# Performance work log

Hardware: AMD Instinct MI355X
Metric: run time of the kernel (lower is better)

Reference implementation:

```python
import jax, jax.numpy as jnp
import numpy as np

N_QUBIT = 22
N_LAYERS = 2
D_LOGICAL = 2  # num_logical_dim (one logical qubit)
DIM = 2 ** N_QUBIT


def _apply_ry(psi, th, q):
    # psi: (B, 2^n) complex64; Ry(th) on qubit q (q=0 is the most significant bit)
    half = th * 0.5
    c = jnp.cos(half).astype(jnp.complex64)
    s = jnp.sin(half).astype(jnp.complex64)
    psi4 = psi.reshape(psi.shape[0], 2 ** q, 2, -1)
    p0, p1 = psi4[:, :, 0], psi4[:, :, 1]
    out = jnp.stack([c * p0 - s * p1, s * p0 + c * p1], axis=2)
    return out.reshape(psi.shape)


def _apply_cnot(psi, c, t):
    a, b = (c, t) if c < t else (t, c)
    right = 2 ** (N_QUBIT - b - 1)
    mid = 2 ** (b - a - 1)
    psi6 = psi.reshape(psi.shape[0], 2 ** a, 2, mid, 2, right)
    if c < t:
        # control is axis 2; flip target axis 4 where control==1
        psi6 = psi6.at[:, :, 1, :, :, :].set(psi6[:, :, 1, :, ::-1, :])
    else:
        # control is axis 4; flip target axis 2 where control==1
        psi6 = psi6.at[:, :, :, :, 1, :].set(psi6[:, :, ::-1, :, 1, :])
    return psi6.reshape(psi.shape)


def _apply_pauli(psi, p, q):
    psi4 = psi.reshape(psi.shape[0], 2 ** q, 2, -1)
    p0, p1 = psi4[:, :, 0], psi4[:, :, 1]
    if p == 'X':
        out = jnp.stack([p1, p0], axis=2)
    elif p == 'Y':
        out = jnp.stack([-1j * p1, 1j * p0], axis=2)
    else:  # Z
        out = jnp.stack([p0, -p1], axis=2)
    return out.reshape(psi.shape)


def _encode(theta):
    # q0[i, i] = 1 for the logical basis states, then run the circuit
    psi = jnp.zeros((D_LOGICAL, DIM), jnp.complex64)
    psi = psi.at[jnp.arange(D_LOGICAL), jnp.arange(D_LOGICAL)].set(1.0)
    for l in range(N_LAYERS):
        for q in range(N_QUBIT):
            psi = _apply_ry(psi, theta[l, q], q)
        for q in range(N_QUBIT):
            psi = _apply_cnot(psi, q, (q + 1) % N_QUBIT)
    return psi


def _kl_loss(theta):
    psi = _encode(theta)  # (D_LOGICAL, 2^n)
    # Knill-Laflamme inner products T_e[i,j] = <psi_i| E_e |psi_j> for all weight-1 Paulis
    Ts = []
    for q in range(N_QUBIT):
        for p in ('X', 'Y', 'Z'):
            epsi = _apply_pauli(psi, p, q)
            Ts.append(jnp.einsum('is,js->ij', psi.conj(), epsi))
    T = jnp.stack(Ts)  # (3*N_QUBIT, D_LOGICAL, D_LOGICAL)
    diag = jnp.diagonal(T, axis1=1, axis2=2)
    lam = diag.mean(axis=1)  # per-error lambda_e
    res = T - lam[:, None, None] * jnp.eye(D_LOGICAL, dtype=T.dtype)
    # loss_type == 'L2'
    return jnp.sum(jnp.abs(res) ** 2)


def setup_inputs() -> dict:
    key = jax.random.key(0)
    theta = jax.random.normal(key, (N_LAYERS, N_QUBIT), dtype=jnp.float32)
    return {"theta": theta}


def reference(theta):
    return _kl_loss(theta)
```

## Files before the change

### kernel.cpp

```cpp
#include <hip/hip_runtime.h>

#define NQ 22
#define DIMN (1u << NQ)

#define PG_OFF 0u
#define PM_OFF 6144u
#define PL_OFF 14336u
#define PF_OFF 126976u
#define CNT_OFF 135168u

struct MaskSet {
    unsigned L[NQ];
    unsigned Linv[NQ];
    unsigned xm[NQ];
    unsigned zm[NQ];
    unsigned frowHi[5];
};

constexpr MaskSet buildMasks() {
    MaskSet M{};
    for (int b = 0; b < NQ; ++b) M.L[b] = 1u << b;
    for (int q = 0; q < NQ; ++q) {
        int bc = NQ - 1 - q, bt = NQ - 1 - ((q + 1) % NQ);
        M.L[bt] ^= M.L[bc];
    }
    unsigned mat[NQ] = {}, aug[NQ] = {};
    for (int b = 0; b < NQ; ++b) { mat[b] = M.L[b]; aug[b] = 1u << b; }
    for (int col = 0; col < NQ; ++col) {
        int piv = col;
        while (!((mat[piv] >> col) & 1u)) ++piv;
        unsigned tm = mat[piv]; mat[piv] = mat[col]; mat[col] = tm;
        unsigned ta = aug[piv]; aug[piv] = aug[col]; aug[col] = ta;
        for (int r = 0; r < NQ; ++r)
            if (r != col && ((mat[r] >> col) & 1u)) { mat[r] ^= mat[col]; aug[r] ^= aug[col]; }
    }
    for (int b = 0; b < NQ; ++b) M.Linv[b] = aug[b];
    for (int j = 0; j < NQ; ++j) {
        int b = NQ - 1 - j;
        unsigned xmv = 0;
        for (int r = 0; r < NQ; ++r)
            if ((aug[r] >> b) & 1u) xmv |= 1u << r;
        M.xm[j] = xmv;
        M.zm[j] = M.L[b];
    }
    for (int j = 0; j < 5; ++j) {
        unsigned f = 0;
        for (int r = 0; r < NQ; ++r)
            if ((aug[r] >> (17 + j)) & 1u) f |= 1u << r;
        M.frowHi[j] = f;
    }
    return M;
}
constexpr int topbit_c(unsigned v) { int b = 0; while (v >> (b + 1)) ++b; return b; }
constexpr unsigned unionHi() {
    MaskSet M = buildMasks();
    unsigned u = 0;
    for (int j = 0; j < 5; ++j) u |= M.frowHi[j];
    return u;
}
static_assert((unionHi() & 0xFFFFu) == 0, "frowHi must only touch bits 16..21");

constexpr unsigned orbGen(int which) {
    MaskSet M = buildMasks();
    return (which == 0 ? M.xm[0] : which == 1 ? M.xm[4] : M.xm[9]) >> 2;
}
constexpr int orbS21() {
    MaskSet M = buildMasks();
    unsigned GA = M.xm[0] >> 2, GB = M.xm[4] >> 2, GC = M.xm[9] >> 2;
    unsigned GQ = M.xm[21] >> 2;
    for (int s = 1; s < 8; ++s) {
        unsigned c = ((s & 1) ? GA : 0u) ^ ((s & 2) ? GB : 0u) ^ ((s & 4) ? GC : 0u);
        if (c == GQ) return s;
    }
    return -1;
}
constexpr bool orbitOK() {
    unsigned GA = orbGen(0), GB = orbGen(1), GC = orbGen(2);
    int cA = topbit_c(GA), cB = topbit_c(GB), cC = topbit_c(GC);
    if (!(cC < cB && cB < cA) || cA > 19) return false;
    if (((GA >> cB) & 1u) || ((GA >> cC) & 1u)) return false;
    if (((GB >> cA) & 1u) || ((GB >> cC) & 1u)) return false;
    if (((GC >> cA) & 1u) || ((GC >> cB) & 1u)) return false;
    return orbS21() > 0;
}
static_assert(orbitOK(), "orbit structure for fused slice measurement must hold");

constexpr bool lowPlanOK() {
    MaskSet M = buildMasks();
    if ((M.xm[10] & ~0xE00u) != 0) return false;
    if ((M.xm[11] & ~0xE00u) != 0) return false;
    for (int q = 12; q <= 19; ++q) {
        if ((M.xm[q] & 3u) != 0 && (M.xm[q] & 3u) != 2u) return false;
        if ((M.zm[q] & 3u) != 0) return false;
        if (topbit_c(M.xm[q]) < 2 || topbit_c(M.xm[q]) > 9) return false;
    }
    if (M.xm[20] != 3u) return false;
    if ((M.zm[20] & 3u) != 2u) return false;
    return true;
}
static_assert(lowPlanOK(), "k_low measurement plan must hold");

__device__ __forceinline__ float fflip(float v, unsigned sbit31) {
    return __int_as_float(__float_as_int(v) ^ (int)sbit31);
}
__device__ __forceinline__ unsigned ph4(unsigned g) { return g ^ ((g >> 6) & 3u); }

__device__ __forceinline__ unsigned sA(unsigned i) {
    return i ^ ((i >> 3) & 7u) ^ (((i >> 6) & 3u) << 3);
}

__device__ __forceinline__ float fold4(float a, float b, float c, float d, int lane) {
    bool p0 = (lane & 1) != 0;
    float kL = p0 ? b : a, sL = p0 ? a : b;
    kL += __shfl_xor(sL, 1);
    float kH = p0 ? d : c, sH = p0 ? c : d;
    kH += __shfl_xor(sH, 1);
    bool p1 = (lane & 2) != 0;
    float k2 = p1 ? kH : kL, s2 = p1 ? kL : kH;
    k2 += __shfl_xor(s2, 2);
    k2 += __shfl_xor(k2, 4);
    k2 += __shfl_xor(k2, 8);
    k2 += __shfl_xor(k2, 16);
    k2 += __shfl_xor(k2, 32);
    return k2;
}

__device__ __forceinline__ void buildTrig(float* trig, const float* __restrict__ theta, int t) {
    if (t < 2 * NQ) {
        int l = t / NQ, q = t % NQ, b = NQ - 1 - q;
        float h = 0.5f * theta[t];
        trig[l * 2 * NQ + b]      = cosf(h);
        trig[l * 2 * NQ + NQ + b] = sinf(h);
    }
}

__device__ __forceinline__ void gates3(float* a, float* b, const float* trig, int b0) {
#pragma unroll
    for (int g = 0; g < 3; ++g) {
        float c = trig[2 * NQ + b0 + g], s = trig[3 * NQ + b0 + g];
#pragma unroll
        for (int e = 0; e < 8; ++e) {
            if (!(e & (1 << g))) {
                int e1 = e | (1 << g);
                float x0 = a[e], x1 = a[e1];
                a[e] = c * x0 - s * x1; a[e1] = s * x0 + c * x1;
                float y0 = b[e], y1 = b[e1];
                b[e] = c * y0 - s * y1; b[e1] = s * y0 + c * y1;
            }
        }
    }
}

__device__ __forceinline__ int slotOf(int s) {
    if (s < 12)  return 4 + s;
    if (s < 28)  return 8 + s;
    if (s < 248) {
        int r = (s - 28) >> 1;
        return (r < 44) ? (40 + r) : (88 + (r - 44));
    }
    int j = s - 248;
    const int b4[4] = { 0, 16, 36, 84 };
    return b4[j >> 2] + (j & 3);
}

__global__ __launch_bounds__(256, 1) void k_genHi(float* __restrict__ phi,
                                                  const float* __restrict__ theta,
                                                  float* __restrict__ P) {
    constexpr MaskSet M = buildMasks();
    __shared__ float red[4 * 12];
    __shared__ float trig[4 * NQ];
    if (blockIdx.x == 0 && threadIdx.x == 0) *(int*)(P + CNT_OFF) = 0;
    buildTrig(trig, theta, threadIdx.x);
    __syncthreads();
    unsigned base = blockIdx.x * 256u + threadIdx.x;
    unsigned P0 = 0;
#pragma unroll
    for (int b = 0; b < NQ; ++b)
        P0 |= ((unsigned)__popc(base & M.Linv[b]) & 1u) << b;
    float pc = 1.f;
#pragma unroll
    for (int b = 1; b < 16; ++b) {
        float cvb = trig[b], svb = trig[NQ + b];
        pc *= ((P0 >> b) & 1u) ? svb : cvb;
    }
    float cv0 = trig[0], sv0 = trig[NQ];
    float C0 = pc * ((P0 & 1u) ? sv0 : cv0);
    float C1 = pc * ((P0 & 1u) ? cv0 : -sv0);
    float cb[6], sb[6];
#pragma unroll
    for (int k = 0; k < 6; ++k) { cb[k] = trig[16 + k]; sb[k] = trig[NQ + 16 + k]; }
    unsigned u0 = P0 >> 16;
    float v0[32], v1[32];
#pragma unroll
    for (int e = 0; e < 32; ++e) {
        unsigned F = 0;
        if (e & 1)  F ^= M.frowHi[0];
        if (e & 2)  F ^= M.frowHi[1];
        if (e & 4)  F ^= M.frowHi[2];
        if (e & 8)  F ^= M.frowHi[3];
        if (e & 16) F ^= M.frowHi[4];
        unsigned u = u0 ^ (F >> 16);
        float vp = (u & 1u) ? sb[0] : cb[0];
#pragma unroll
        for (int k = 1; k < 6; ++k) vp *= ((u >> k) & 1u) ? sb[k] : cb[k];
        v0[e] = vp * C0;
        v1[e] = vp * C1;
    }
    float c2[5], s2[5];
#pragma unroll
    for (int j = 0; j < 5; ++j) {
        c2[j] = trig[2 * NQ + 17 + j];
        s2[j] = trig[3 * NQ + 17 + j];
    }
#pragma unroll
    for (int j = 0; j < 5; ++j) {
#pragma unroll
        for (int e = 0; e < 32; ++e) {
            if (!(e & (1 << j))) {
                int e1 = e | (1 << j);
                float a0 = v0[e], a1 = v0[e1];
                v0[e]  = c2[j] * a0 - s2[j] * a1;
                v0[e1] = s2[j] * a0 + c2[j] * a1;
                float b0 = v1[e], b1 = v1[e1];
                v1[e]  = c2[j] * b0 - s2[j] * b1;
                v1[e1] = s2[j] * b0 + c2[j] * b1;
            }
        }
    }
#pragma unroll
    for (int e = 0; e < 32; ++e) {
        unsigned a = base | ((unsigned)e << 17);
        phi[a] = v0[e];
        phi[DIMN + a] = v1[e];
    }
    int lane = threadIdx.x & 63, w = threadIdx.x >> 6;
#pragma unroll
    for (int i = 1; i <= 3; ++i) {
        unsigned ex  = M.xm[i] >> 17;
        unsigned zme = M.zm[i] >> 17;
        float t00 = 0.f, t11 = 0.f, t01 = 0.f, u01 = 0.f;
#pragma unroll
        for (int e = 0; e < 32; ++e) {
            int ep = e ^ (int)ex;
            t00 += v0[e] * v0[ep];
            t11 += v1[e] * v1[ep];
            float p = v0[e] * v1[ep];
            t01 += p;
            unsigned sg = ((unsigned)__popc((unsigned)ep & zme) & 1u) << 31;
            u01 += fflip(p, sg);
        }
        float r = fold4(t00, t11, t01, u01, lane);
        if (lane < 4) red[w * 12 + (i - 1) * 4 + lane] = r;
    }
    __syncthreads();
    int t = threadIdx.x;
    if (t < 12) {
        float r = red[t] + red[12 + t] + red[24 + t] + red[36 + t];
        P[PG_OFF + (unsigned)t * 512u + blockIdx.x] = r;
    }
}

__global__ __launch_bounds__(256, 1) void k_midA(float* __restrict__ phi,
                                                 const float* __restrict__ theta,
                                                 float* __restrict__ P) {
    constexpr MaskSet M = buildMasks();
    __shared__ float red[4 * 16];
    __shared__ float trig[4 * NQ];
    buildTrig(trig, theta, threadIdx.x);
    __syncthreads();
    unsigned tid = blockIdx.x * 256u + threadIdx.x;
    unsigned base = (tid & 0xFFFu) | ((tid >> 12) << 17);
    float v0[32], v1[32];
#pragma unroll
    for (int e = 0; e < 32; ++e) {
        unsigned a = base | ((unsigned)e << 12);
        v0[e] = phi[a];
        v1[e] = phi[DIMN + a];
    }
    float c[5], s[5];
#pragma unroll
    for (int j = 0; j < 5; ++j) {
        c[j] = trig[2 * NQ + 12 + j];
        s[j] = trig[3 * NQ + 12 + j];
    }
#pragma unroll
    for (int j = 0; j < 5; ++j) {
#pragma unroll
        for (int e = 0; e < 32; ++e) {
            if (!(e & (1 << j))) {
                int e1 = e | (1 << j);
                float a0 = v0[e], a1 = v0[e1];
                v0[e]  = c[j] * a0 - s[j] * a1;
                v0[e1] = s[j] * a0 + c[j] * a1;
                float b0 = v1[e], b1 = v1[e1];
                v1[e]  = c[j] * b0 - s[j] * b1;
                v1[e1] = s[j] * b0 + c[j] * b1;
            }
        }
    }
#pragma unroll
    for (int e = 0; e < 32; ++e) {
        unsigned a = base | ((unsigned)e << 12);
        phi[a] = v0[e];
        phi[DIMN + a] = v1[e];
    }
    int lane = threadIdx.x & 63, w = threadIdx.x >> 6;
#pragma unroll
    for (int i = 5; i <= 8; ++i) {
        unsigned ex  = (M.xm[i] >> 12) & 31u;
        unsigned zme = (M.zm[i] >> 12) & 31u;
        unsigned bs31 = ((unsigned)__popc(base & M.zm[i]) & 1u) << 31;
        float t00 = 0.f, t11 = 0.f, t01 = 0.f, u01 = 0.f;
#pragma unroll
        for (int e = 0; e < 32; ++e) {
            int ep = e ^ (int)ex;
            t00 += v0[e] * v0[ep];
            t11 += v1[e] * v1[ep];
            float p = v0[e] * v1[ep];
            t01 += p;
            unsigned sg = ((unsigned)__popc((unsigned)ep & zme) & 1u) << 31;
            u01 += fflip(p, sg ^ bs31);
        }
        float r = fold4(t00, t11, t01, u01, lane);
        if (lane < 4) red[w * 16 + (i - 5) * 4 + lane] = r;
    }
    __syncthreads();
    int t = threadIdx.x;
    if (t < 16) {
        float r = red[t] + red[16 + t] + red[32 + t] + red[48 + t];
        P[PM_OFF + (unsigned)t * 512u + blockIdx.x] = r;
    }
}

__global__ __launch_bounds__(512, 4) void k_low(float* __restrict__ phi,
                                                const float* __restrict__ theta,
                                                float* __restrict__ P) {
    constexpr MaskSet M = buildMasks();
    __shared__ float As[4096];
    __shared__ float Bs[4096];
    __shared__ float redZ[8 * 33];
    __shared__ float redQ[8 * 44];
    __shared__ float trig[4 * NQ];
    float4* As4 = (float4*)As;
    float4* Bs4 = (float4*)Bs;
    int t = threadIdx.x;
    int lane = t & 63, w = t >> 6;
    unsigned base = blockIdx.x * 4096u;
    float a[8], b[8];
    buildTrig(trig, theta, t);

    {
        const float4* g0 = (const float4*)(phi + base);
        const float4* g1 = (const float4*)(phi + DIMN + base);
        float4 va0 = g0[2 * t], va1 = g0[2 * t + 1];
        float4 vb0 = g1[2 * t], vb1 = g1[2 * t + 1];
        a[0] = va0.x; a[1] = va0.y; a[2] = va0.z; a[3] = va0.w;
        a[4] = va1.x; a[5] = va1.y; a[6] = va1.z; a[7] = va1.w;
        b[0] = vb0.x; b[1] = vb0.y; b[2] = vb0.z; b[3] = vb0.w;
        b[4] = vb1.x; b[5] = vb1.y; b[6] = vb1.z; b[7] = vb1.w;
        __syncthreads();
        gates3(a, b, trig, 0);
#pragma unroll
        for (int j = 0; j < 8; ++j) {
            unsigned i = ((unsigned)t << 3) | (unsigned)j;
            unsigned A = sA(i);
            As[A] = a[j]; Bs[A] = b[j];
        }
    }
    __syncthreads();

    {
#pragma unroll
        for (int j = 0; j < 8; ++j) {
            unsigned i = (((unsigned)t >> 3) << 6) | ((unsigned)j << 3) | ((unsigned)t & 7u);
            unsigned A = sA(i);
            a[j] = As[A]; b[j] = Bs[A];
        }
        gates3(a, b, trig, 3);
#pragma unroll
        for (int j = 0; j < 8; ++j) {
            unsigned i = (((unsigned)t >> 3) << 6) | ((unsigned)j << 3) | ((unsigned)t & 7u);
            unsigned A = sA(i);
            As[A] = a[j]; Bs[A] = b[j];
        }
    }
    __syncthreads();

    {
#pragma unroll
        for (int j = 0; j < 8; ++j) {
            unsigned i = (((unsigned)t >> 6) << 9) | ((unsigned)j << 6) | ((unsigned)t & 63u);
            unsigned A = sA(i);
            a[j] = As[A]; b[j] = Bs[A];
        }
        gates3(a, b, trig, 6);
#pragma unroll
        for (int j = 0; j < 8; ++j) {
            unsigned i = (((unsigned)t >> 6) << 9) | ((unsigned)j << 6) | ((unsigned)t & 63u);
            unsigned A = sA(i);
            As[A] = a[j]; Bs[A] = b[j];
        }
    }
    __syncthreads();

    {
#pragma unroll
        for (int j = 0; j < 8; ++j) {
            unsigned i = ((unsigned)j << 9) | (unsigned)t;
            unsigned A = sA(i);
            a[j] = As[A]; b[j] = Bs[A];
        }
        gates3(a, b, trig, 9);
    }
    __syncthreads();

#pragma unroll
    for (int j = 0; j < 8; ++j) {
        unsigned i = ((unsigned)j << 9) | (unsigned)t;
        phi[base + i] = a[j];
        phi[DIMN + base + i] = b[j];
        unsigned p = i ^ (((i >> 8) & 3u) << 2);
        As[p] = a[j]; Bs[p] = b[j];
    }

#pragma unroll
    for (int c = 0; c < 3; ++c) {
        float p[8];
#pragma unroll
        for (int j = 0; j < 8; ++j)
            p[j] = (c == 0) ? a[j] * a[j] : (c == 1) ? b[j] * b[j] : a[j] * b[j];
        float s1[4], d1[4];
#pragma unroll
        for (int j = 0; j < 4; ++j) { s1[j] = p[j] + p[j + 4]; d1[j] = p[j] - p[j + 4]; }
        float s2_0 = s1[0] + s1[2], s2_1 = s1[1] + s1[3];
        float d2_0 = d1[0] - d1[2], d2_1 = d1[1] - d1[3];
        float SS = s2_0 + s2_1;
        float z0 = (d1[0] + d1[1]) + (d1[2] + d1[3]);
        float z1 = d2_0 + d2_1;
        float d3 = d2_0 - d2_1;
        float r = fold4(SS, z0, z1, 0.f, lane);
        if (lane < 3) redZ[w * 33 + c * 11 + lane] = r;
        float v = d3;
#pragma unroll
        for (int s = 0; s < 6; ++s) {
            float u = __shfl_xor(v, 1 << s);
            v = u + fflip(v, ((unsigned)(lane >> s) & 1u) << 31);
        }
        int pcnt = __popc(lane);
        if (lane == 64 - (64 >> pcnt)) redZ[w * 33 + c * 11 + 3 + pcnt] = v;
    }
    __syncthreads();

    if (t < 66) {
        int c = t % 3, q = t / 3;
        int idx, wm;
        if (q == 0 || q == 21)      { idx = 9; wm = 7; }
        else if (q <= 9)            { idx = 0; wm = 0; }
        else if (q == 10)           { idx = 1; wm = 0; }
        else if (q == 11)           { idx = 2; wm = 0; }
        else if (q == 12)           { idx = 3; wm = 0; }
        else if (q == 13)           { idx = 3; wm = 4; }
        else if (q == 14)           { idx = 3; wm = 6; }
        else if (q == 15)           { idx = 3; wm = 7; }
        else                        { idx = q - 12; wm = 7; }
        float val = 0.f;
#pragma unroll
        for (int ww = 0; ww < 8; ++ww) {
            float rv = redZ[ww * 33 + c * 11 + idx];
            val += ((__popc(ww & wm) & 1) ? -rv : rv);
        }
        unsigned sg = (unsigned)__popc(base & M.zm[q]) & 1u;
        P[PL_OFF + (44u + (unsigned)t) * 1024u + blockIdx.x] = sg ? -val : val;
    }

#pragma unroll
    for (int i = 0; i < 2; ++i) {
        int q = 10 + i;
        unsigned je  = (M.xm[q] >> 9) & 7u;
        unsigned zmj = (M.zm[q] >> 9) & 7u;
        unsigned zb31 = ((unsigned)__popc(base & M.zm[q]) & 1u) << 31;
        float t00 = 0.f, t11 = 0.f, t01 = 0.f, u01 = 0.f;
#pragma unroll
        for (int j = 0; j < 8; ++j) {
            int jp = j ^ (int)je;
            t00 += a[j] * a[jp];
            t11 += b[j] * b[jp];
            float p = a[j] * b[jp];
            t01 += p;
            unsigned sg = ((unsigned)__popc((unsigned)jp & zmj) & 1u) << 31;
            u01 += fflip(p, sg ^ zb31);
        }
        float r = fold4(t00, t11, t01, u01, lane);
        if (lane < 4) redQ[w * 44 + 4 * i + lane] = r;
    }

#pragma unroll
    for (int iq = 2; iq < 10; ++iq) {
        int q = 10 + iq;
        unsigned m = M.xm[q], zm = M.zm[q];
        unsigned zb = (unsigned)__popc(base & zm) & 1u;
        int gb = topbit_c(M.xm[q]) - 2;
        unsigned mg4 = m >> 2;
        unsigned swap2 = m & 3u;
        float t00 = 0.f, t11 = 0.f, t01 = 0.f, u01 = 0.f;
        unsigned gc = (unsigned)t;
        unsigned g = ((gc >> gb) << (gb + 1)) | (gc & ((1u << gb) - 1u));
        unsigned gx = g ^ mg4;
        float4 a0 = As4[ph4(g)],  a1 = Bs4[ph4(g)];
        float4 b0 = As4[ph4(gx)], b1 = Bs4[ph4(gx)];
        if (swap2) {
            b0 = make_float4(b0.z, b0.w, b0.x, b0.y);
            b1 = make_float4(b1.z, b1.w, b1.x, b1.y);
        }
        unsigned szg = ((unsigned)__popc((g << 2) & zm) + zb) & 1u;
        unsigned szx = ((unsigned)__popc((gx << 2) & zm) + zb) & 1u;
        unsigned fg = szg << 31, fx = szx << 31;
        const float* A0 = &a0.x; const float* A1 = &a1.x;
        const float* B0 = &b0.x; const float* B1 = &b1.x;
#pragma unroll
        for (int j = 0; j < 4; ++j) {
            t00 += A0[j] * B0[j];
            t11 += A1[j] * B1[j];
            float p = A0[j] * B1[j], r2 = B0[j] * A1[j];
            t01 += p + r2;
            u01 += fflip(p, fx) + fflip(r2, fg);
        }
        t00 *= 2.f; t11 *= 2.f;
        float r = fold4(t00, t11, t01, u01, lane);
        if (lane < 4) redQ[w * 44 + 4 * iq + lane] = r;
    }
    {
        unsigned zm = M.zm[20];
        unsigned zb = (unsigned)__popc(base & zm) & 1u;
        float t00 = 0.f, t11 = 0.f, t01 = 0.f, u01 = 0.f;
#pragma unroll
        for (int k = 0; k < 2; ++k) {
            unsigned g = (unsigned)t + 512u * k;
            float4 a0 = As4[ph4(g)], a1 = Bs4[ph4(g)];
            unsigned szg = ((unsigned)__popc((g << 2) & zm) + zb) & 1u;
            const float* A0 = &a0.x; const float* A1 = &a1.x;
#pragma unroll
            for (int j = 0; j < 4; ++j) {
                int jx = j ^ 3;
                float p = A0[j] * A0[jx];
                float q2 = A1[j] * A1[jx];
                float cr = A0[j] * A1[jx];
                t00 += p; t11 += q2; t01 += cr;
                unsigned sj = ((unsigned)(jx >> 1) & 1u) ^ szg;
                u01 += fflip(cr, sj << 31);
            }
        }
        float r = fold4(t00, t11, t01, u01, lane);
        if (lane < 4) redQ[w * 44 + 40 + lane] = r;
    }
    __syncthreads();
    if (t < 44) {
        float r = 0.f;
#pragma unroll
        for (int ww = 0; ww < 8; ++ww) r += redQ[ww * 44 + t];
        P[PL_OFF + (unsigned)t * 1024u + blockIdx.x] = r;
    }
}

__global__ __launch_bounds__(256) void k_measF(const float* __restrict__ phi,
                                               float* __restrict__ P,
                                               float* __restrict__ out) {
    constexpr MaskSet M = buildMasks();
    constexpr unsigned GA = orbGen(0), GB = orbGen(1), GC = orbGen(2);
    constexpr int pc0 = topbit_c(GC), pc1 = topbit_c(GB), pc2 = topbit_c(GA);
    __shared__ float red[4 * 16];
    __shared__ float accv[160];
    __shared__ int lastBlk;
    unsigned t = blockIdx.x * 256u + threadIdx.x;
    unsigned g = t;
    g = ((g >> pc0) << (pc0 + 1)) | (g & ((1u << pc0) - 1u));
    g = ((g >> pc1) << (pc1 + 1)) | (g & ((1u << pc1) - 1u));
    g = ((g >> pc2) << (pc2 + 1)) | (g & ((1u << pc2) - 1u));
    const float4* P0 = (const float4*)phi;
    const float4* P1 = (const float4*)(phi + DIMN);
    unsigned idx[8];
    float4 u4[8], w4[8];
#pragma unroll
    for (int s = 0; s < 8; ++s) {
        idx[s] = g ^ ((s & 1) ? GA : 0u) ^ ((s & 2) ? GB : 0u) ^ ((s & 4) ? GC : 0u);
        u4[s] = P0[idx[s]];
        w4[s] = P1[idx[s]];
    }
    constexpr int QN[4] = { 0, 4, 9, 21 };
    constexpr int SX[4] = { 1, 2, 4, orbS21() };
    float res[16];
#pragma unroll
    for (int qi = 0; qi < 4; ++qi) {
        const unsigned xq = M.xm[QN[qi]];
        const unsigned zq = M.zm[QN[qi]];
        const int sx = SX[qi];
        const int mu = (int)(xq & 3u);
        const unsigned zh = zq >> 2, zl = zq & 3u;
        unsigned fz[8];
#pragma unroll
        for (int s = 0; s < 8; ++s)
            fz[s] = ((unsigned)__popc(idx[s] & zh) & 1u) << 31;
        unsigned pj31[4];
#pragma unroll
        for (int j = 0; j < 4; ++j)
            pj31[j] = ((unsigned)__popc((unsigned)j & zl) & 1u) << 31;
        float t00 = 0.f, t11 = 0.f, t01 = 0.f, u01 = 0.f;
#pragma unroll
        for (int s = 0; s < 8; ++s) {
            const int s2 = s ^ sx;
            const float* A0 = &u4[s].x;
            const float* A1 = &w4[s].x;
            const float* B0 = &u4[s2].x;
            const float* B1 = &w4[s2].x;
            const unsigned fe = fz[s2];
#pragma unroll
            for (int j = 0; j < 4; ++j) {
                const int jp = j ^ mu;
                t00 += A0[j] * B0[jp];
                t11 += A1[j] * B1[jp];
                float p = A0[j] * B1[jp];
                t01 += p;
                u01 += fflip(p, fe ^ pj31[jp]);
            }
        }
        res[4 * qi + 0] = t00; res[4 * qi + 1] = t11;
        res[4 * qi + 2] = t01; res[4 * qi + 3] = u01;
    }
    int lane = threadIdx.x & 63, w = threadIdx.x >> 6;
#pragma unroll
    for (int g4 = 0; g4 < 4; ++g4) {
        float r = fold4(res[4 * g4 + 0], res[4 * g4 + 1], res[4 * g4 + 2], res[4 * g4 + 3], lane);
        if (lane < 4) red[w * 16 + 4 * g4 + lane] = r;
    }
    __syncthreads();
    int tt = threadIdx.x;
    if (tt < 16) {
        float r = red[tt] + red[16 + tt] + red[32 + tt] + red[48 + tt];
        P[PF_OFF + (unsigned)tt * 512u + blockIdx.x] = r;
    }
    __threadfence();
    __syncthreads();
    if (tt == 0) {
        int c = atomicAdd((int*)(P + CNT_OFF), 1);
        lastBlk = (c == (int)gridDim.x - 1);
    }
    __syncthreads();
    if (!lastBlk) return;
    __threadfence();

    if (tt < 160) accv[tt] = 0.f;
    __syncthreads();
    {
        const float4* Pf = (const float4*)P;
        int ngroups = (w < 3) ? 17 : 15;
        for (int gi = 0; gi < ngroups; ++gi) {
            int s0 = w * 68 + gi * 4;
            float q[4];
#pragma unroll
            for (int k = 0; k < 4; ++k) {
                const float4* sp = Pf + (unsigned)(s0 + k) * 128u;
                float4 x = sp[lane];
                float4 y = sp[lane + 64];
                q[k] = ((x.x + x.y) + (x.z + x.w)) + ((y.x + y.y) + (y.z + y.w));
            }
            float r = fold4(q[0], q[1], q[2], q[3], lane);
            if (lane < 4) atomicAdd(&accv[slotOf(s0 + lane)], r);
        }
    }
    __syncthreads();
    float v = 0.f;
    if (tt < NQ) {
        float t00 = accv[4 * tt], t11 = accv[4 * tt + 1];
        float t01 = accv[4 * tt + 2], u01 = accv[4 * tt + 3];
        float d = t00 - t11;
        v = 0.5f * d * d + 2.f * t01 * t01 + 2.f * u01 * u01;
    } else if (tt < 2 * NQ) {
        int q = tt - NQ;
        float z0 = accv[88 + 3 * q], z1 = accv[88 + 3 * q + 1];
        float zz = accv[88 + 3 * q + 2];
        float d = z0 - z1;
        v = 0.5f * d * d + 2.f * zz * zz;
    }
    v += __shfl_down(v, 32); v += __shfl_down(v, 16); v += __shfl_down(v, 8);
    v += __shfl_down(v, 4);  v += __shfl_down(v, 2);  v += __shfl_down(v, 1);
    if (tt == 0) out[0] = v;
}

extern "C" void kernel_launch(void* const* d_in, const int* in_sizes, int n_in,
                              void* d_out, int out_size, void* d_ws, size_t ws_size,
                              hipStream_t stream) {
    const float* theta = (const float*)d_in[0];
    float* out  = (float*)d_out;
    float* ws   = (float*)d_ws;
    float* phi  = ws;
    float* P    = ws + 2 * (size_t)DIMN;

    k_genHi<<<512, 256, 0, stream>>>(phi, theta, P);
    k_midA<<<512, 256, 0, stream>>>(phi, theta, P);
    k_low<<<1024, 512, 0, stream>>>(phi, theta, P);
    k_measF<<<512, 256, 0, stream>>>(phi, P, out);
}
```

Measured before the change: 176.5 us.

## Replace orbit-fused measurement with per-qubit pair passes in k_measF

The fused 8-point orbit measurement kernel is replaced by separate pair-wise passes for qubits 0/21, 4 and 9. Each pass loads a state element and its Pauli partner, exploits symmetry to cover half the pairs and doubles the diagonal terms. The grid is doubled to 1024 blocks, and the partial-sum layout and final reduction indexing are adjusted to match. This lowers register pressure and raises parallelism, at the cost of reading the state vector three times instead of once.

```diff
diff --git a/kernel.cpp b/kernel.cpp
--- a/kernel.cpp
+++ b/kernel.cpp
@@ -7,7 +7,7 @@
 #define PM_OFF 6144u
 #define PL_OFF 14336u
 #define PF_OFF 126976u
-#define CNT_OFF 135168u
+#define CNT_OFF 143360u
 
 struct MaskSet {
     unsigned L[NQ];
@@ -60,30 +60,19 @@
 }
 static_assert((unionHi() & 0xFFFFu) == 0, "frowHi must only touch bits 16..21");
 
-constexpr unsigned orbGen(int which) {
+constexpr bool measPlanOK() {
     MaskSet M = buildMasks();
-    return (which == 0 ? M.xm[0] : which == 1 ? M.xm[4] : M.xm[9]) >> 2;
-}
-constexpr int orbS21() {
-    MaskSet M = buildMasks();
-    unsigned GA = M.xm[0] >> 2, GB = M.xm[4] >> 2, GC = M.xm[9] >> 2;
-    unsigned GQ = M.xm[21] >> 2;
-    for (int s = 1; s < 8; ++s) {
-        unsigned c = ((s & 1) ? GA : 0u) ^ ((s & 2) ? GB : 0u) ^ ((s & 4) ? GC : 0u);
-        if (c == GQ) return s;
-    }
-    return -1;
-}
-constexpr bool orbitOK() {
-    unsigned GA = orbGen(0), GB = orbGen(1), GC = orbGen(2);
-    int cA = topbit_c(GA), cB = topbit_c(GB), cC = topbit_c(GC);
-    if (!(cC < cB && cB < cA) || cA > 19) return false;
-    if (((GA >> cB) & 1u) || ((GA >> cC) & 1u)) return false;
-    if (((GB >> cA) & 1u) || ((GB >> cC) & 1u)) return false;
-    if (((GC >> cA) & 1u) || ((GC >> cB) & 1u)) return false;
-    return orbS21() > 0;
-}
-static_assert(orbitOK(), "orbit structure for fused slice measurement must hold");
+    if ((M.xm[0] >> 2) != (M.xm[21] >> 2)) return false;
+    if ((M.xm[0] & 3u) != 0u) return false;
+    if ((M.xm[21] & 3u) != 1u) return false;
+    if ((M.xm[4] & 3u) != 0u) return false;
+    if ((M.xm[9] & 3u) != 0u) return false;
+    if (topbit_c(M.xm[0] >> 2) != 19) return false;
+    if (topbit_c(M.xm[4] >> 2) != 15) return false;
+    if (topbit_c(M.xm[9] >> 2) != 10) return false;
+    return true;
+}
+static_assert(measPlanOK(), "measF pass plan must hold");
 
 constexpr bool lowPlanOK() {
     MaskSet M = buildMasks();
@@ -158,9 +147,35 @@
         int r = (s - 28) >> 1;
         return (r < 44) ? (40 + r) : (88 + (r - 44));
     }
-    int j = s - 248;
-    const int b4[4] = { 0, 16, 36, 84 };
-    return b4[j >> 2] + (j & 3);
+    int j = (s - 248) >> 1;
+    int qi = j >> 2;
+    int b4 = (qi == 0) ? 0 : (qi == 1) ? 16 : (qi == 2) ? 36 : 84;
+    return b4 + (j & 3);
+}
+
+__device__ __forceinline__ void accPair(float4 a0, float4 a1, float4 b0in, float4 b1in,
+                                        unsigned g, unsigned gx, unsigned ml2, unsigned zm,
+                                        float* acc) {
+    float4 b0 = b0in, b1 = b1in;
+    if (ml2) {
+        b0 = make_float4(b0.y, b0.x, b0.w, b0.z);
+        b1 = make_float4(b1.y, b1.x, b1.w, b1.z);
+    }
+    unsigned zl = zm & 3u;
+    unsigned fg = (((unsigned)__popc((g  << 2) & zm) & 1u) << 31);
+    unsigned fx = (((unsigned)__popc((gx << 2) & zm) & 1u) << 31);
+    const float* A0 = &a0.x; const float* A1 = &a1.x;
+    const float* B0 = &b0.x; const float* B1 = &b1.x;
+#pragma unroll
+    for (int j = 0; j < 4; ++j) {
+        unsigned pg31 = (((unsigned)__popc((unsigned)j & zl) & 1u) << 31);
+        unsigned px31 = (((unsigned)__popc(((unsigned)j ^ ml2) & zl) & 1u) << 31);
+        acc[0] += A0[j] * B0[j];
+        acc[1] += A1[j] * B1[j];
+        float p = A0[j] * B1[j], r = B0[j] * A1[j];
+        acc[2] += p + r;
+        acc[3] += fflip(p, fx ^ px31) + fflip(r, fg ^ pg31);
+    }
 }
 
 __global__ __launch_bounds__(256, 1) void k_genHi(float* __restrict__ phi,
@@ -566,67 +581,62 @@
                                                float* __restrict__ P,
                                                float* __restrict__ out) {
     constexpr MaskSet M = buildMasks();
-    constexpr unsigned GA = orbGen(0), GB = orbGen(1), GC = orbGen(2);
-    constexpr int pc0 = topbit_c(GC), pc1 = topbit_c(GB), pc2 = topbit_c(GA);
     __shared__ float red[4 * 16];
     __shared__ float accv[160];
     __shared__ int lastBlk;
-    unsigned t = blockIdx.x * 256u + threadIdx.x;
-    unsigned g = t;
-    g = ((g >> pc0) << (pc0 + 1)) | (g & ((1u << pc0) - 1u));
-    g = ((g >> pc1) << (pc1 + 1)) | (g & ((1u << pc1) - 1u));
-    g = ((g >> pc2) << (pc2 + 1)) | (g & ((1u << pc2) - 1u));
     const float4* P0 = (const float4*)phi;
     const float4* P1 = (const float4*)(phi + DIMN);
-    unsigned idx[8];
-    float4 u4[8], w4[8];
-#pragma unroll
-    for (int s = 0; s < 8; ++s) {
-        idx[s] = g ^ ((s & 1) ? GA : 0u) ^ ((s & 2) ? GB : 0u) ^ ((s & 4) ? GC : 0u);
-        u4[s] = P0[idx[s]];
-        w4[s] = P1[idx[s]];
-    }
-    constexpr int QN[4] = { 0, 4, 9, 21 };
-    constexpr int SX[4] = { 1, 2, 4, orbS21() };
+    unsigned tid = blockIdx.x * 256u + threadIdx.x;
+    int lane = threadIdx.x & 63, w = threadIdx.x >> 6;
     float res[16];
 #pragma unroll
-    for (int qi = 0; qi < 4; ++qi) {
-        const unsigned xq = M.xm[QN[qi]];
-        const unsigned zq = M.zm[QN[qi]];
-        const int sx = SX[qi];
-        const int mu = (int)(xq & 3u);
-        const unsigned zh = zq >> 2, zl = zq & 3u;
-        unsigned fz[8];
-#pragma unroll
-        for (int s = 0; s < 8; ++s)
-            fz[s] = ((unsigned)__popc(idx[s] & zh) & 1u) << 31;
-        unsigned pj31[4];
-#pragma unroll
-        for (int j = 0; j < 4; ++j)
-            pj31[j] = ((unsigned)__popc((unsigned)j & zl) & 1u) << 31;
-        float t00 = 0.f, t11 = 0.f, t01 = 0.f, u01 = 0.f;
-#pragma unroll
-        for (int s = 0; s < 8; ++s) {
-            const int s2 = s ^ sx;
-            const float* A0 = &u4[s].x;
-            const float* A1 = &w4[s].x;
-            const float* B0 = &u4[s2].x;
-            const float* B1 = &w4[s2].x;
-            const unsigned fe = fz[s2];
-#pragma unroll
-            for (int j = 0; j < 4; ++j) {
-                const int jp = j ^ mu;
-                t00 += A0[j] * B0[jp];
-                t11 += A1[j] * B1[jp];
-                float p = A0[j] * B1[jp];
-                t01 += p;
-                u01 += fflip(p, fe ^ pj31[jp]);
-            }
-        }
-        res[4 * qi + 0] = t00; res[4 * qi + 1] = t11;
-        res[4 * qi + 2] = t01; res[4 * qi + 3] = u01;
-    }
-    int lane = threadIdx.x & 63, w = threadIdx.x >> 6;
+    for (int k = 0; k < 16; ++k) res[k] = 0.f;
+
+    {
+        constexpr unsigned mg4 = 0xC0000u;
+        constexpr unsigned zm0 = buildMasks().zm[0];
+        constexpr unsigned zm21 = buildMasks().zm[21];
+#pragma unroll
+        for (int k = 0; k < 2; ++k) {
+            unsigned g = tid + (unsigned)k * 262144u;
+            unsigned gx = g ^ mg4;
+            float4 a0 = P0[g], a1 = P1[g];
+            float4 b0 = P0[gx], b1 = P1[gx];
+            accPair(a0, a1, b0, b1, g, gx, 0u, zm0,  &res[0]);
+            accPair(a0, a1, b0, b1, g, gx, 1u, zm21, &res[12]);
+        }
+        res[0] *= 2.f; res[1] *= 2.f;
+        res[12] *= 2.f; res[13] *= 2.f;
+    }
+    {
+        constexpr unsigned mg4 = 0xC000u;
+        constexpr unsigned zm4 = buildMasks().zm[4];
+#pragma unroll
+        for (int k = 0; k < 2; ++k) {
+            unsigned pc = tid + (unsigned)k * 262144u;
+            unsigned g = ((pc >> 15) << 16) | (pc & 0x7FFFu);
+            unsigned gx = g ^ mg4;
+            float4 a0 = P0[g], a1 = P1[g];
+            float4 b0 = P0[gx], b1 = P1[gx];
+            accPair(a0, a1, b0, b1, g, gx, 0u, zm4, &res[4]);
+        }
+        res[4] *= 2.f; res[5] *= 2.f;
+    }
+    {
+        constexpr unsigned mg4 = 0x600u;
+        constexpr unsigned zm9 = buildMasks().zm[9];
+#pragma unroll
+        for (int k = 0; k < 2; ++k) {
+            unsigned pc = tid + (unsigned)k * 262144u;
+            unsigned g = ((pc >> 10) << 11) | (pc & 0x3FFu);
+            unsigned gx = g ^ mg4;
+            float4 a0 = P0[g], a1 = P1[g];
+            float4 b0 = P0[gx], b1 = P1[gx];
+            accPair(a0, a1, b0, b1, g, gx, 0u, zm9, &res[8]);
+        }
+        res[8] *= 2.f; res[9] *= 2.f;
+    }
+
 #pragma unroll
     for (int g4 = 0; g4 < 4; ++g4) {
         float r = fold4(res[4 * g4 + 0], res[4 * g4 + 1], res[4 * g4 + 2], res[4 * g4 + 3], lane);
@@ -636,7 +646,7 @@
     int tt = threadIdx.x;
     if (tt < 16) {
         float r = red[tt] + red[16 + tt] + red[32 + tt] + red[48 + tt];
-        P[PF_OFF + (unsigned)tt * 512u + blockIdx.x] = r;
+        P[PF_OFF + (unsigned)tt * 1024u + blockIdx.x] = r;
     }
     __threadfence();
     __syncthreads();
@@ -652,9 +662,10 @@
     __syncthreads();
     {
         const float4* Pf = (const float4*)P;
-        int ngroups = (w < 3) ? 17 : 15;
-        for (int gi = 0; gi < ngroups; ++gi) {
-            int s0 = w * 68 + gi * 4;
+        int g0w = (w < 2) ? w * 18 : 36 + (w - 2) * 17;
+        int ng  = (w < 2) ? 18 : 17;
+        for (int gi = 0; gi < ng; ++gi) {
+            int s0 = (g0w + gi) * 4;
             float q[4];
 #pragma unroll
             for (int k = 0; k < 4; ++k) {
@@ -698,5 +709,5 @@
     k_genHi<<<512, 256, 0, stream>>>(phi, theta, P);
     k_midA<<<512, 256, 0, stream>>>(phi, theta, P);
     k_low<<<1024, 512, 0, stream>>>(phi, theta, P);
-    k_measF<<<512, 256, 0, stream>>>(phi, P, out);
-}
+    k_measF<<<1024, 256, 0, stream>>>(phi, P, out);
+}
```

Result: slower. 248.7 us (+40.9%).
